# Kernel tuning notes

Hardware: AMD Instinct MI355X
Metric: run time of the kernel (lower is better)

The kernel has to match this reference:

```python
import jax, jax.numpy as jnp
import numpy as np

EPS = 1e-5

def _layer_norm(x, g, b):
    mu = jnp.mean(x, axis=-1, keepdims=True)
    var = jnp.mean((x - mu) ** 2, axis=-1, keepdims=True)
    return (x - mu) * jax.lax.rsqrt(var + EPS) * g + b

def _lstm(x, w_ih, w_hh, b_ih, b_hh):
    # x: [B,T,I]; w_ih: [4H,I]; w_hh: [4H,H]; gate order i,f,g,o (torch)
    B, T, _ = x.shape
    H = w_hh.shape[1]
    xg = jnp.einsum('bti,gi->btg', x, w_ih) + b_ih + b_hh  # [B,T,4H]
    def step(carry, xt):
        h, c = carry
        g = xt + h @ w_hh.T
        i, f, gg, o = jnp.split(g, 4, axis=-1)
        i = jax.nn.sigmoid(i); f = jax.nn.sigmoid(f)
        gg = jnp.tanh(gg); o = jax.nn.sigmoid(o)
        c = f * c + i * gg
        h = o * jnp.tanh(c)
        return (h, c), h
    h0 = jnp.zeros((B, H), x.dtype)
    (_, _), hs = jax.lax.scan(step, (h0, h0), jnp.swapaxes(xg, 0, 1))
    return jnp.swapaxes(hs, 0, 1)  # [B,T,H]

def _gru(x, w_ih, w_hh, b_ih, b_hh):
    # gate order r,z,n (torch); n uses r * (W_hn h + b_hn)
    B, T, _ = x.shape
    H = w_hh.shape[1]
    xg = jnp.einsum('bti,gi->btg', x, w_ih) + b_ih  # [B,T,3H]
    def step(h, xt):
        hg = h @ w_hh.T + b_hh
        xr, xz, xn = jnp.split(xt, 3, axis=-1)
        hr, hz, hn = jnp.split(hg, 3, axis=-1)
        r = jax.nn.sigmoid(xr + hr)
        z = jax.nn.sigmoid(xz + hz)
        n = jnp.tanh(xn + r * hn)
        h = (1.0 - z) * n + z * h
        return h, h
    h0 = jnp.zeros((B, H), x.dtype)
    _, hs = jax.lax.scan(step, h0, jnp.swapaxes(xg, 0, 1))
    return jnp.swapaxes(hs, 0, 1)

def _rnn_tanh(x, w_ih, w_hh, b_ih, b_hh):
    B, T, _ = x.shape
    H = w_hh.shape[1]
    xg = jnp.einsum('bti,gi->btg', x, w_ih) + b_ih + b_hh
    def step(h, xt):
        h = jnp.tanh(xt + h @ w_hh.T)
        return h, h
    h0 = jnp.zeros((B, H), x.dtype)
    _, hs = jax.lax.scan(step, h0, jnp.swapaxes(xg, 0, 1))
    return jnp.swapaxes(hs, 0, 1)

def setup_inputs() -> dict:
    key = jax.random.key(0)
    B, T, I, H, O = 32, 1024, 256, 512, 1000
    ks = jax.random.split(key, 16)
    s_lstm = 1.0 / np.sqrt(H)
    def u(k, shape, s):
        return jax.random.uniform(k, shape, jnp.float32, -s, s)
    return {
        'x': jax.random.normal(ks[0], (B, T, I), jnp.float32),
        'lstm_w_ih': u(ks[1], (4 * H, I), s_lstm),
        'lstm_w_hh': u(ks[2], (4 * H, H), s_lstm),
        'lstm_b_ih': u(ks[3], (4 * H,), s_lstm),
        'lstm_b_hh': u(ks[4], (4 * H,), s_lstm),
        'ln1_g': jnp.ones((H,), jnp.float32),
        'ln1_b': jnp.zeros((H,), jnp.float32),
        'gru_w_ih': u(ks[5], (3 * H, H), s_lstm),
        'gru_w_hh': u(ks[6], (3 * H, H), s_lstm),
        'gru_b_ih': u(ks[7], (3 * H,), s_lstm),
        'gru_b_hh': u(ks[8], (3 * H,), s_lstm),
        'ln2_g': jnp.ones((H,), jnp.float32),
        'ln2_b': jnp.zeros((H,), jnp.float32),
        'rnn_w_ih': u(ks[9], (H, H), s_lstm),
        'rnn_w_hh': u(ks[10], (H, H), s_lstm),
        'rnn_b_ih': u(ks[11], (H,), s_lstm),
        'rnn_b_hh': u(ks[12], (H,), s_lstm),
        'fc_w': u(ks[13], (O, H), s_lstm),
        'fc_b': u(ks[14], (O,), s_lstm),
    }

def reference(x, lstm_w_ih, lstm_w_hh, lstm_b_ih, lstm_b_hh, ln1_g, ln1_b,
              gru_w_ih, gru_w_hh, gru_b_ih, gru_b_hh, ln2_g, ln2_b,
              rnn_w_ih, rnn_w_hh, rnn_b_ih, rnn_b_hh, fc_w, fc_b):
    h = _lstm(x, lstm_w_ih, lstm_w_hh, lstm_b_ih, lstm_b_hh)
    h = _layer_norm(h, ln1_g, ln1_b)
    h = _gru(h, gru_w_ih, gru_w_hh, gru_b_ih, gru_b_hh)
    h = _layer_norm(h, ln2_g, ln2_b)
    h = _rnn_tanh(h, rnn_w_ih, rnn_w_hh, rnn_b_ih, rnn_b_hh)
    h = h[:, -1]  # [B,H]
    return h @ fc_w.T + fc_b  # [B,O]
```

## Files before the change

### kernel.cpp

```cpp
#include <hip/hip_runtime.h>
#include <stdint.h>

#define T_SEQ 1024
#define BATCH 32
#define HID   512
#define RING  32

typedef unsigned short u16;
typedef unsigned long long u64;
typedef short bf16x8 __attribute__((ext_vector_type(8)));
typedef float f32x4  __attribute__((ext_vector_type(4)));
typedef unsigned int u32x4 __attribute__((ext_vector_type(4)));

#define CAN64 0x7FC07FC07FC07FC0ull

__device__ __forceinline__ float bf2f(u16 u) {
  union { unsigned u; float f; } v; v.u = ((unsigned)u) << 16; return v.f;
}
__device__ __forceinline__ u16 f2bf(float f) {
  union { float f; unsigned u; } v; v.f = f;
  unsigned r = v.u + 0x7fffu + ((v.u >> 16) & 1u);
  return (u16)(r >> 16);
}
__device__ __forceinline__ float sigf(float x) { return 1.0f / (1.0f + __expf(-x)); }
__device__ __forceinline__ float tanh_fast(float x) { return 2.0f * sigf(2.0f * x) - 1.0f; }

__device__ __forceinline__ void st_dev(u64* p, u64 v) {
  __hip_atomic_store(p, v, __ATOMIC_RELAXED, __HIP_MEMORY_SCOPE_AGENT);
}
__device__ __forceinline__ int ld_flag(const int* p) {
  return __hip_atomic_load(p, __ATOMIC_RELAXED, __HIP_MEMORY_SCOPE_AGENT);
}

#define GLD16(dst, p, OFS) \
  asm volatile("global_load_dwordx4 %0, %1, off offset:" OFS " sc0 sc1" \
               : "=v"(dst) : "v"(p) : "memory")
#define GST16(p, val, OFS) \
  asm volatile("global_store_dwordx4 %0, %1, off offset:" OFS " sc0 sc1" \
               :: "v"(p), "v"(val) : "memory")

struct Frag {
  u32x4 d0,d1,d2,d3,d4,d5,d6,d7,d8,d9,d10,d11,d12,d13,d14,d15;
};

__device__ __forceinline__ void issue_frag(const u16* p, Frag& f) {
  GLD16(f.d0,  p, "0");   GLD16(f.d1,  p, "64");
  GLD16(f.d2,  p, "128"); GLD16(f.d3,  p, "192");
  GLD16(f.d4,  p, "256"); GLD16(f.d5,  p, "320");
  GLD16(f.d6,  p, "384"); GLD16(f.d7,  p, "448");
  GLD16(f.d8,  p, "512"); GLD16(f.d9,  p, "576");
  GLD16(f.d10, p, "640"); GLD16(f.d11, p, "704");
  GLD16(f.d12, p, "768"); GLD16(f.d13, p, "832");
  GLD16(f.d14, p, "896"); GLD16(f.d15, p, "960");
}

__device__ __forceinline__ bool chk16(u32x4 q) {
  union { u32x4 q; u64 h[2]; } u; u.q = q;
  return (u.h[0] != CAN64) & (u.h[1] != CAN64);
}
__device__ __forceinline__ bool frag_ok(const Frag& f) {
  bool ok = chk16(f.d0);
  ok &= chk16(f.d1);  ok &= chk16(f.d2);  ok &= chk16(f.d3);
  ok &= chk16(f.d4);  ok &= chk16(f.d5);  ok &= chk16(f.d6);
  ok &= chk16(f.d7);  ok &= chk16(f.d8);  ok &= chk16(f.d9);
  ok &= chk16(f.d10); ok &= chk16(f.d11); ok &= chk16(f.d12);
  ok &= chk16(f.d13); ok &= chk16(f.d14); ok &= chk16(f.d15);
  return ok;
}

__device__ __forceinline__ f32x4 frag_compute(const Frag& f, const u16 (*w)[520],
                                              int wrow, int kq) {
  f32x4 z = {0.f,0.f,0.f,0.f};
  f32x4 a[4] = {z, z, z, z};
#define FSTEP(ii, dd) { union { u32x4 q; bf16x8 v; } c; c.q = f.dd; \
  bf16x8 bv = *reinterpret_cast<const bf16x8*>(&w[wrow][kq + ii * 32]); \
  a[ii & 3] = __builtin_amdgcn_mfma_f32_16x16x32_bf16(c.v, bv, a[ii & 3], 0, 0, 0); }
  FSTEP(0,d0)   FSTEP(1,d1)   FSTEP(2,d2)   FSTEP(3,d3)
  FSTEP(4,d4)   FSTEP(5,d5)   FSTEP(6,d6)   FSTEP(7,d7)
  FSTEP(8,d8)   FSTEP(9,d9)   FSTEP(10,d10) FSTEP(11,d11)
  FSTEP(12,d12) FSTEP(13,d13) FSTEP(14,d14) FSTEP(15,d15)
#undef FSTEP
  return (a[0] + a[1]) + (a[2] + a[3]);
}

__device__ __forceinline__ int poll_min(const int* base, int n, int lane) {
  int f = 0x7fffffff;
  if (lane < n) f = ld_flag(&base[lane]);
#pragma unroll
  for (int off = 32; off >= 1; off >>= 1) {
    int o = __shfl_xor(f, off);
    f = o < f ? o : f;
  }
  return f;
}

__global__ __launch_bounds__(256) void cast_f32_bf16(const float* __restrict__ in,
                                                     u16* __restrict__ out, int n) {
  int i = (blockIdx.x * 256 + threadIdx.x) * 8;
  if (i + 7 < n) {
    float4 v0 = *reinterpret_cast<const float4*>(in + i);
    float4 v1 = *reinterpret_cast<const float4*>(in + i + 4);
    uint4 o;
    o.x = (unsigned)f2bf(v0.x) | ((unsigned)f2bf(v0.y) << 16);
    o.y = (unsigned)f2bf(v0.z) | ((unsigned)f2bf(v0.w) << 16);
    o.z = (unsigned)f2bf(v1.x) | ((unsigned)f2bf(v1.y) << 16);
    o.w = (unsigned)f2bf(v1.z) | ((unsigned)f2bf(v1.w) << 16);
    *reinterpret_cast<uint4*>(out + i) = o;
  } else {
    for (; i < n; ++i) out[i] = f2bf(in[i]);
  }
}

__global__ __launch_bounds__(256) void fill_canary(u64* __restrict__ p, long n) {
  long i = (long)blockIdx.x * 256 + threadIdx.x;
  if (i < n) p[i] = CAN64;
}

__global__ __launch_bounds__(256) void gemm_xg(
    const u16* __restrict__ A, const u16* __restrict__ W,
    const float* __restrict__ bias1, const float* __restrict__ bias2,
    u16* __restrict__ out, int N, int K, int strideB, int strideT)
{
  __shared__ u16 As[64][72];
  __shared__ u16 Bs[64][72];
  int tid  = threadIdx.x;
  int lane = tid & 63;
  int wave = tid >> 6;
  int m0 = blockIdx.x * 64;
  int n0 = blockIdx.y * 64;

  f32x4 zero = {0.f, 0.f, 0.f, 0.f};
  f32x4 acc[4] = {zero, zero, zero, zero};

  int srow = tid >> 2;
  int scol = (tid & 3) * 16;

  int m_s = m0 + srow;
  long arow = (long)(m_s & (BATCH - 1)) * strideB + (long)(m_s >> 5) * strideT;
  const u16* aptr = A + arow * K + scol;
  const u16* wptr = W + (long)(n0 + srow) * K + scol;

  for (int kk = 0; kk < K; kk += 64) {
    __syncthreads();
    uint4 a0 = *reinterpret_cast<const uint4*>(aptr + kk);
    uint4 a1 = *reinterpret_cast<const uint4*>(aptr + kk + 8);
    uint4 b0 = *reinterpret_cast<const uint4*>(wptr + kk);
    uint4 b1 = *reinterpret_cast<const uint4*>(wptr + kk + 8);
    *reinterpret_cast<uint4*>(&As[srow][scol])     = a0;
    *reinterpret_cast<uint4*>(&As[srow][scol + 8]) = a1;
    *reinterpret_cast<uint4*>(&Bs[srow][scol])     = b0;
    *reinterpret_cast<uint4*>(&Bs[srow][scol + 8]) = b1;
    __syncthreads();
    int am = wave * 16 + (lane & 15);
    int kq = (lane >> 4) * 8;
#pragma unroll
    for (int ks = 0; ks < 2; ++ks) {
      bf16x8 af = *reinterpret_cast<const bf16x8*>(&As[am][kq + ks * 32]);
#pragma unroll
      for (int nb = 0; nb < 4; ++nb) {
        bf16x8 bf = *reinterpret_cast<const bf16x8*>(&Bs[nb * 16 + (lane & 15)][kq + ks * 32]);
        acc[nb] = __builtin_amdgcn_mfma_f32_16x16x32_bf16(af, bf, acc[nb], 0, 0, 0);
      }
    }
  }
  int quad = lane >> 4;
#pragma unroll
  for (int nb = 0; nb < 4; ++nb) {
    int n = n0 + nb * 16 + (lane & 15);
    float bv = bias1[n] + (bias2 ? bias2[n] : 0.0f);
    int g = n >> 9, k = n & 511;
#pragma unroll
    for (int r = 0; r < 4; ++r) {
      int m = m0 + wave * 16 + quad * 4 + r;
      int t = m >> 5, b = m & (BATCH - 1);
      out[(((long)t * BATCH + b) * HID + k) * 4 + g] = f2bf(acc[nb][r] + bv);
    }
  }
}

template <int ROLE>
__device__ void recur_role(
    int wg, const u16* __restrict__ xg, const u16* __restrict__ up,
    const u16* __restrict__ wih, const u16* __restrict__ whh,
    const float* __restrict__ bih, const float* __restrict__ bhh,
    u16* __restrict__ hist, int* fl_own,
    const int* cons, int n_cons,
    u16 (*w_lds)[520], float (*gx)[33], float (*gh)[33], u16 (*hs)[8])
{
  constexpr int NG = (ROLE == 0) ? 4 : (ROLE == 1) ? 3 : 1;
  constexpr int NPAD = (ROLE == 2) ? 16 : 32;
  constexpr int XROWS = (ROLE > 0) ? NG * 8 : 0;
  constexpr int TOT = XROWS + NG * 8;
  int tid = threadIdx.x, lane = tid & 63, wave = tid >> 6;
  int hbase = wg * 8;

  for (int idx = tid; idx < TOT * 64; idx += 256) {
    int row = idx >> 6, chunk = idx & 63;
    int n = (row < XROWS) ? row : (row - XROWS);
    const u16* src = (row < XROWS) ? wih : whh;
    int g = n >> 3, dd = n & 7;
    uint4 v = *reinterpret_cast<const uint4*>(src + ((long)(g * 512 + hbase + dd)) * 512 + chunk * 8);
    *reinterpret_cast<uint4*>(&w_lds[row][chunk * 8]) = v;
  }
  __syncthreads();

  int mt = wave & 1, nt = wave >> 1;
  bool mact = (nt * 16) < NPAD;
  int colw = nt * 16 + (lane & 15);
  int wr = (colw < NG * 8) ? colw : (NG * 8 - 1);
  int arow = mt * 16 + (lane & 15);
  int kq = (lane >> 4) * 8;
  float bxw = 0.f, bhw = 0.f;
  if (colw < NG * 8) {
    int g = colw >> 3, dd = colw & 7;
    if constexpr (ROLE == 1) { bxw = bih[g * 512 + hbase + dd]; bhw = bhh[g * 512 + hbase + dd]; }
    if constexpr (ROLE == 2) { bxw = bih[hbase + dd] + bhh[hbase + dd]; }
    (void)g;
  }
  int b_c = tid >> 3, d_c = tid & 7;
  float c_st = 0.f, h_st = 0.f;
  int ccache = 0;

  for (int t = 0; t < T_SEQ; ++t) {
    u64 xq = 0;
    if constexpr (ROLE == 0)
      xq = *reinterpret_cast<const u64*>(xg + (((long)t * BATCH + b_c) * HID + hbase + d_c) * 4);

    f32x4 aX = {0.f,0.f,0.f,0.f}, aH = {0.f,0.f,0.f,0.f};
    if (mact) {
      if (wave == 0) {
        if (cons != nullptr && t >= RING - 1) {
          int need = t - (RING - 2);
          while (ccache < need) {
            ccache = poll_min(cons, n_cons, lane);
            if (ccache < need) __builtin_amdgcn_s_sleep(8);
          }
        }
        int pb = lane >> 1, half = lane & 1;
        st_dev(reinterpret_cast<u64*>(
                   hist + (((long)((t + 1) & (RING - 1)) * BATCH + pb) * HID + hbase + half * 4)),
               CAN64);
      }
      Frag fX, fH;
      bool okX = (ROLE == 0), okH = (t == 0);
      const u16* pX = nullptr;
      if constexpr (ROLE > 0)
        pX = up + ((long)(t & (RING - 1)) * BATCH + arow) * HID + kq;
      const u16* pH = hist + ((long)((t - 1) & (RING - 1)) * BATCH + arow) * HID + kq;
      while (!(okX & okH)) {
        if (!okX) issue_frag(pX, fX);
        if (!okH) issue_frag(pH, fH);
        asm volatile("s_waitcnt vmcnt(0)" ::: "memory");
        __builtin_amdgcn_sched_barrier(0);
        if (!okX) okX = (bool)__all(frag_ok(fX));
        if (!okH) okH = (bool)__all(frag_ok(fH));
      }
      if constexpr (ROLE > 0) aX = frag_compute(fX, w_lds, wr, kq);
      if (t > 0)              aH = frag_compute(fH, w_lds + XROWS, wr, kq);

      int quad = lane >> 4;
#pragma unroll
      for (int r = 0; r < 4; ++r) {
        int row = mt * 16 + quad * 4 + r;
        gx[row][colw] = aX[r] + bxw;
        gh[row][colw] = aH[r] + bhw;
      }
    }
    __syncthreads();

    float hnew;
    if constexpr (ROLE == 0) {
      float xv0 = bf2f((u16)(xq));
      float xv1 = bf2f((u16)(xq >> 16));
      float xv2 = bf2f((u16)(xq >> 32));
      float xv3 = bf2f((u16)(xq >> 48));
      float h0 = gh[b_c][0 * 8 + d_c];
      float h1 = gh[b_c][1 * 8 + d_c];
      float h2 = gh[b_c][2 * 8 + d_c];
      float h3 = gh[b_c][3 * 8 + d_c];
      float ig = sigf(xv0 + h0), fg = sigf(xv1 + h1);
      float gg = tanh_fast(xv2 + h2), og = sigf(xv3 + h3);
      c_st = fg * c_st + ig * gg;
      hnew = og * tanh_fast(c_st);
    } else if constexpr (ROLE == 1) {
      float xr_ = gx[b_c][0 * 8 + d_c], xz = gx[b_c][1 * 8 + d_c], xn = gx[b_c][2 * 8 + d_c];
      float hr  = gh[b_c][0 * 8 + d_c], hz = gh[b_c][1 * 8 + d_c], hn = gh[b_c][2 * 8 + d_c];
      float r = sigf(xr_ + hr), z = sigf(xz + hz);
      float n = tanh_fast(xn + r * hn);
      hnew = (1.f - z) * n + z * h_st;
      h_st = hnew;
    } else {
      hnew = tanh_fast(gx[b_c][d_c] + gh[b_c][d_c]);
    }
    hs[b_c][d_c] = f2bf(hnew);
    __syncthreads();

    if (wave == 0) {
      asm volatile("s_waitcnt vmcnt(0)" ::: "memory");
      int pb = lane >> 1, half = lane & 1;
      u64 val = *reinterpret_cast<const u64*>(&hs[pb][half * 4]);
      st_dev(reinterpret_cast<u64*>(
                 hist + (((long)(t & (RING - 1)) * BATCH + pb) * HID + hbase + half * 4)),
             val);
      if (tid == 0 && fl_own != nullptr)
        __hip_atomic_store(&fl_own[wg], t + 1, __ATOMIC_RELAXED, __HIP_MEMORY_SCOPE_AGENT);
    }
  }
}

__device__ void ln_role(int wg, const u16* __restrict__ in, u16* __restrict__ out,
                        const float* __restrict__ gv, const float* __restrict__ bv,
                        int* fl_out, const int* cons, int n_cons)
{
  int tid = threadIdx.x, lane = tid & 63, wave = tid >> 6;
  int row = wg * 8 + wave * 2 + (lane >> 5);
  int l32 = lane & 31, k0 = l32 * 16;
  float gr[16], br[16];
#pragma unroll
  for (int j = 0; j < 16; ++j) { gr[j] = gv[k0 + j]; br[j] = bv[k0 + j]; }
  int ccache = 0;
  u32x4 canv = {0x7FC07FC0u, 0x7FC07FC0u, 0x7FC07FC0u, 0x7FC07FC0u};

  for (int t = 0; t < T_SEQ; ++t) {
    if (t >= RING - 1) {
      int need = t - (RING - 2);
      while (ccache < need) {
        ccache = poll_min(cons, n_cons, lane);
        if (ccache < need) __builtin_amdgcn_s_sleep(8);
      }
    }
    u16* pc = out + ((long)((t + 1) & (RING - 1)) * BATCH + row) * HID + k0;
    GST16(pc, canv, "0");
    GST16(pc, canv, "16");

    const u16* p = in + ((long)(t & (RING - 1)) * BATCH + row) * HID + k0;
    u32x4 q0, q1;
    bool ok;
    do {
      GLD16(q0, p, "0");
      GLD16(q1, p, "16");
      asm volatile("s_waitcnt vmcnt(0)" ::: "memory");
      __builtin_amdgcn_sched_barrier(0);
      ok = (bool)__all(chk16(q0) & chk16(q1));
    } while (!ok);

    union { u32x4 q; u16 s[8]; } u0, u1;
    u0.q = q0; u1.q = q1;
    float x[16];
#pragma unroll
    for (int i = 0; i < 8; ++i) { x[i] = bf2f(u0.s[i]); x[8 + i] = bf2f(u1.s[i]); }
    float s = 0.f, s2 = 0.f;
#pragma unroll
    for (int i = 0; i < 16; ++i) { s += x[i]; s2 += x[i] * x[i]; }
#pragma unroll
    for (int off = 1; off < 32; off <<= 1) { s += __shfl_xor(s, off); s2 += __shfl_xor(s2, off); }
    float mu = s * (1.f / 512.f);
    float var = s2 * (1.f / 512.f) - mu * mu;
    float rs = rsqrtf(var + 1e-5f);
    union { u16 o[16]; u32x4 q[2]; } ov;
#pragma unroll
    for (int i = 0; i < 16; ++i) ov.o[i] = f2bf((x[i] - mu) * rs * gr[i] + br[i]);
    u16* po = out + ((long)(t & (RING - 1)) * BATCH + row) * HID + k0;
    GST16(po, ov.q[0], "0");
    GST16(po, ov.q[1], "16");
    __syncthreads();
    if (tid == 0)
      __hip_atomic_store(&fl_out[wg], t + 1, __ATOMIC_RELAXED, __HIP_MEMORY_SCOPE_AGENT);
  }
}

__global__ __launch_bounds__(256, 1) void fused_kernel(
    const u16* __restrict__ xg, const u16* __restrict__ lstm_whh,
    const u16* __restrict__ gru_wih, const u16* __restrict__ gru_whh,
    const float* __restrict__ gru_bih, const float* __restrict__ gru_bhh,
    const u16* __restrict__ rnn_wih, const u16* __restrict__ rnn_whh,
    const float* __restrict__ rnn_bih, const float* __restrict__ rnn_bhh,
    const float* __restrict__ ln1_g, const float* __restrict__ ln1_b,
    const float* __restrict__ ln2_g, const float* __restrict__ ln2_b,
    u16* h1, u16* ln1o, u16* h2, u16* ln2o, u16* h3, int* fl)
{
  __shared__ u16 w_lds[48][520];
  __shared__ float gx[32][33];
  __shared__ float gh[32][33];
  __shared__ u16 hs[32][8];
  int bid = blockIdx.x;
  if (bid < 64)
    recur_role<0>(bid, xg, nullptr, nullptr, lstm_whh, nullptr, nullptr,
                  h1, nullptr, fl + 64, 4, w_lds, gx, gh, hs);
  else if (bid < 68)
    ln_role(bid - 64, h1, ln1o, ln1_g, ln1_b, fl + 64, fl + 128, 64);
  else if (bid < 132)
    recur_role<1>(bid - 68, nullptr, ln1o, gru_wih, gru_whh, gru_bih, gru_bhh,
                  h2, fl + 128, fl + 192, 4, w_lds, gx, gh, hs);
  else if (bid < 136)
    ln_role(bid - 132, h2, ln2o, ln2_g, ln2_b, fl + 192, fl + 256, 64);
  else
    recur_role<2>(bid - 136, nullptr, ln2o, rnn_wih, rnn_whh, rnn_bih, rnn_bhh,
                  h3, fl + 256, nullptr, 0, w_lds, gx, gh, hs);
}

__global__ __launch_bounds__(256) void fc_kernel(
    const u16* __restrict__ hlast, const u16* __restrict__ w,
    const float* __restrict__ bias, float* __restrict__ out)
{
  int tg = blockIdx.x * 256 + threadIdx.x;
  if (tg >= BATCH * 1000) return;
  int b = tg / 1000, o = tg % 1000;
  const u16* hp = hlast + (long)b * HID;
  const u16* wp = w + (long)o * HID;
  float acc = 0.f;
  for (int k = 0; k < HID; k += 8) {
    uint4 hu = *reinterpret_cast<const uint4*>(hp + k);
    uint4 wu = *reinterpret_cast<const uint4*>(wp + k);
    u16* hsv = reinterpret_cast<u16*>(&hu);
    u16* wsv = reinterpret_cast<u16*>(&wu);
#pragma unroll
    for (int i = 0; i < 8; ++i) acc += bf2f(hsv[i]) * bf2f(wsv[i]);
  }
  out[tg] = acc + bias[o];
}

__global__ void sentinel_kernel(float* out) { out[0] = 12345.0f; }

extern "C" void kernel_launch(void* const* d_in, const int* in_sizes, int n_in,
                              void* d_out, int out_size, void* d_ws, size_t ws_size,
                              hipStream_t stream)
{
  (void)in_sizes; (void)n_in; (void)out_size;
  const float* x        = (const float*)d_in[0];
  const float* lstm_wih = (const float*)d_in[1];
  const float* lstm_whh = (const float*)d_in[2];
  const float* lstm_bih = (const float*)d_in[3];
  const float* lstm_bhh = (const float*)d_in[4];
  const float* ln1_g    = (const float*)d_in[5];
  const float* ln1_b    = (const float*)d_in[6];
  const float* gru_wih  = (const float*)d_in[7];
  const float* gru_whh  = (const float*)d_in[8];
  const float* gru_bih  = (const float*)d_in[9];
  const float* gru_bhh  = (const float*)d_in[10];
  const float* ln2_g    = (const float*)d_in[11];
  const float* ln2_b    = (const float*)d_in[12];
  const float* rnn_wih  = (const float*)d_in[13];
  const float* rnn_whh  = (const float*)d_in[14];
  const float* rnn_bih  = (const float*)d_in[15];
  const float* rnn_bhh  = (const float*)d_in[16];
  const float* fc_w     = (const float*)d_in[17];
  const float* fc_b     = (const float*)d_in[18];
  float* out = (float*)d_out;

  char* ws = (char*)d_ws;
  size_t off = 0;
  auto alloc = [&](size_t bytes) -> void* {
    void* p = ws + off; off += (bytes + 255) & ~(size_t)255; return p;
  };
  int* flags     = (int*)alloc(320 * sizeof(int));
  u16* xbf       = (u16*)alloc((size_t)BATCH * T_SEQ * 256 * 2);
  u16* lstm_wih_b= (u16*)alloc((size_t)2048 * 256 * 2);
  u16* lstm_whh_b= (u16*)alloc((size_t)2048 * 512 * 2);
  u16* gru_wih_b = (u16*)alloc((size_t)1536 * 512 * 2);
  u16* gru_whh_b = (u16*)alloc((size_t)1536 * 512 * 2);
  u16* rnn_wih_b = (u16*)alloc((size_t)512 * 512 * 2);
  u16* rnn_whh_b = (u16*)alloc((size_t)512 * 512 * 2);
  u16* fc_w_b    = (u16*)alloc((size_t)1000 * 512 * 2);
  u16* xg2       = (u16*)alloc((size_t)T_SEQ * BATCH * HID * 4 * 2);
  u16* h1        = (u16*)alloc((size_t)RING * BATCH * HID * 2);
  u16* ln1o      = (u16*)alloc((size_t)RING * BATCH * HID * 2);
  u16* h2        = (u16*)alloc((size_t)RING * BATCH * HID * 2);
  u16* ln2o      = (u16*)alloc((size_t)RING * BATCH * HID * 2);
  u16* h3        = (u16*)alloc((size_t)RING * BATCH * HID * 2);

  if (off > ws_size) {
    sentinel_kernel<<<1, 1, 0, stream>>>(out);
    return;
  }

  hipMemsetAsync(flags, 0, 320 * sizeof(int), stream);

  const long ncan = 5L * RING * BATCH * HID * 2 / 8;
  fill_canary<<<(int)((ncan + 255) / 256), 256, 0, stream>>>((u64*)h1, ncan);

  auto cast = [&](const float* src, u16* dst, int n) {
    cast_f32_bf16<<<(n + 2047) / 2048, 256, 0, stream>>>(src, dst, n);
  };
  cast(x,        xbf,        BATCH * T_SEQ * 256);
  cast(lstm_wih, lstm_wih_b, 2048 * 256);
  cast(lstm_whh, lstm_whh_b, 2048 * 512);
  cast(gru_wih,  gru_wih_b,  1536 * 512);
  cast(gru_whh,  gru_whh_b,  1536 * 512);
  cast(rnn_wih,  rnn_wih_b,  512 * 512);
  cast(rnn_whh,  rnn_whh_b,  512 * 512);
  cast(fc_w,     fc_w_b,     1000 * 512);

  const int M64 = (BATCH * T_SEQ) / 64;
  gemm_xg<<<dim3(M64, 2048 / 64), 256, 0, stream>>>(
      xbf, lstm_wih_b, lstm_bih, lstm_bhh, xg2, 2048, 256, 1024, 1);

  fused_kernel<<<200, 256, 0, stream>>>(
      xg2, lstm_whh_b,
      gru_wih_b, gru_whh_b, gru_bih, gru_bhh,
      rnn_wih_b, rnn_whh_b, rnn_bih, rnn_bhh,
      ln1_g, ln1_b, ln2_g, ln2_b,
      h1, ln1o, h2, ln2o, h3, flags);

  fc_kernel<<<(BATCH * 1000 + 255) / 256, 256, 0, stream>>>(
      h3 + (size_t)31 * BATCH * HID, fc_w_b, fc_b, out);
}
```

Before: 6.949 ms.

## Split recurrent matmul over K across waves and prefetch next-step input fragment

Reworks the per-step wave decomposition: instead of waves splitting over output columns (with some idle for the RNN role), each wave now takes half of the K dimension and all output columns, and partial sums are reduced through shared memory with an extra barrier. Fragments are halved to 8 loads, and the upstream input fragment for step t+1 is prefetched right after computing step t, so the input load latency overlaps the hidden-state wait. Biases move into the elementwise phase, and the trailing vmcnt wait before publishing h is dropped. Adds an extra __syncthreads and LDS accumulate per step, and relies on the prefetched sentinel check to retry stale data.

After: 6.273 ms. -9.7%, faster.

```diff
diff --git a/kernel.cpp b/kernel.cpp
--- a/kernel.cpp
+++ b/kernel.cpp
@@ -28,59 +28,52 @@
 __device__ __forceinline__ void st_dev(u64* p, u64 v) {
   __hip_atomic_store(p, v, __ATOMIC_RELAXED, __HIP_MEMORY_SCOPE_AGENT);
 }
+__device__ __forceinline__ void st_tag(int* p, int v) {
+  __hip_atomic_store(p, v, __ATOMIC_RELAXED, __HIP_MEMORY_SCOPE_AGENT);
+}
 __device__ __forceinline__ int ld_flag(const int* p) {
   return __hip_atomic_load(p, __ATOMIC_RELAXED, __HIP_MEMORY_SCOPE_AGENT);
 }
 
-#define GLD16(dst, p, OFS) \
+#define GLD16A(dst, p, OFS) \
   asm volatile("global_load_dwordx4 %0, %1, off offset:" OFS " sc0 sc1" \
                : "=v"(dst) : "v"(p) : "memory")
-#define GST16(p, val, OFS) \
+#define GST16A(p, val, OFS) \
   asm volatile("global_store_dwordx4 %0, %1, off offset:" OFS " sc0 sc1" \
                :: "v"(p), "v"(val) : "memory")
 
-struct Frag {
-  u32x4 d0,d1,d2,d3,d4,d5,d6,d7,d8,d9,d10,d11,d12,d13,d14,d15;
-};
-
-__device__ __forceinline__ void issue_frag(const u16* p, Frag& f) {
-  GLD16(f.d0,  p, "0");   GLD16(f.d1,  p, "64");
-  GLD16(f.d2,  p, "128"); GLD16(f.d3,  p, "192");
-  GLD16(f.d4,  p, "256"); GLD16(f.d5,  p, "320");
-  GLD16(f.d6,  p, "384"); GLD16(f.d7,  p, "448");
-  GLD16(f.d8,  p, "512"); GLD16(f.d9,  p, "576");
-  GLD16(f.d10, p, "640"); GLD16(f.d11, p, "704");
-  GLD16(f.d12, p, "768"); GLD16(f.d13, p, "832");
-  GLD16(f.d14, p, "896"); GLD16(f.d15, p, "960");
+struct Frag8 { u32x4 d0,d1,d2,d3,d4,d5,d6,d7; };
+
+__device__ __forceinline__ void issue_frag8A(const u16* p, Frag8& f) {
+  GLD16A(f.d0, p, "0");   GLD16A(f.d1, p, "64");
+  GLD16A(f.d2, p, "128"); GLD16A(f.d3, p, "192");
+  GLD16A(f.d4, p, "256"); GLD16A(f.d5, p, "320");
+  GLD16A(f.d6, p, "384"); GLD16A(f.d7, p, "448");
 }
 
 __device__ __forceinline__ bool chk16(u32x4 q) {
   union { u32x4 q; u64 h[2]; } u; u.q = q;
   return (u.h[0] != CAN64) & (u.h[1] != CAN64);
 }
-__device__ __forceinline__ bool frag_ok(const Frag& f) {
+__device__ __forceinline__ bool frag8_ok(const Frag8& f) {
   bool ok = chk16(f.d0);
-  ok &= chk16(f.d1);  ok &= chk16(f.d2);  ok &= chk16(f.d3);
-  ok &= chk16(f.d4);  ok &= chk16(f.d5);  ok &= chk16(f.d6);
-  ok &= chk16(f.d7);  ok &= chk16(f.d8);  ok &= chk16(f.d9);
-  ok &= chk16(f.d10); ok &= chk16(f.d11); ok &= chk16(f.d12);
-  ok &= chk16(f.d13); ok &= chk16(f.d14); ok &= chk16(f.d15);
+  ok &= chk16(f.d1); ok &= chk16(f.d2); ok &= chk16(f.d3);
+  ok &= chk16(f.d4); ok &= chk16(f.d5); ok &= chk16(f.d6); ok &= chk16(f.d7);
   return ok;
 }
 
-__device__ __forceinline__ f32x4 frag_compute(const Frag& f, const u16 (*w)[520],
-                                              int wrow, int kq) {
-  f32x4 z = {0.f,0.f,0.f,0.f};
-  f32x4 a[4] = {z, z, z, z};
-#define FSTEP(ii, dd) { union { u32x4 q; bf16x8 v; } c; c.q = f.dd; \
-  bf16x8 bv = *reinterpret_cast<const bf16x8*>(&w[wrow][kq + ii * 32]); \
-  a[ii & 3] = __builtin_amdgcn_mfma_f32_16x16x32_bf16(c.v, bv, a[ii & 3], 0, 0, 0); }
-  FSTEP(0,d0)   FSTEP(1,d1)   FSTEP(2,d2)   FSTEP(3,d3)
-  FSTEP(4,d4)   FSTEP(5,d5)   FSTEP(6,d6)   FSTEP(7,d7)
-  FSTEP(8,d8)   FSTEP(9,d9)   FSTEP(10,d10) FSTEP(11,d11)
-  FSTEP(12,d12) FSTEP(13,d13) FSTEP(14,d14) FSTEP(15,d15)
-#undef FSTEP
-  return (a[0] + a[1]) + (a[2] + a[3]);
+template <int NT>
+__device__ __forceinline__ void frag_compute8(const Frag8& f, const u16 (*w)[520],
+                                              int lane, int kq2, int ngr, f32x4* acc) {
+#define HSTEP(ii, dd) { union { u32x4 q; bf16x8 v; } c; c.q = f.dd; \
+  _Pragma("unroll") \
+  for (int n2 = 0; n2 < NT; ++n2) { \
+    int cw = n2 * 16 + (lane & 15); int wr2 = cw < ngr ? cw : ngr - 1; \
+    bf16x8 bv = *reinterpret_cast<const bf16x8*>(&w[wr2][kq2 + ii * 32]); \
+    acc[n2] = __builtin_amdgcn_mfma_f32_16x16x32_bf16(c.v, bv, acc[n2], 0, 0, 0); } }
+  HSTEP(0,d0) HSTEP(1,d1) HSTEP(2,d2) HSTEP(3,d3)
+  HSTEP(4,d4) HSTEP(5,d5) HSTEP(6,d6) HSTEP(7,d7)
+#undef HSTEP
 }
 
 __device__ __forceinline__ int poll_min(const int* base, int n, int lane) {
@@ -187,10 +180,12 @@
     const int* cons, int n_cons,
     u16 (*w_lds)[520], float (*gx)[33], float (*gh)[33], u16 (*hs)[8])
 {
-  constexpr int NG = (ROLE == 0) ? 4 : (ROLE == 1) ? 3 : 1;
-  constexpr int NPAD = (ROLE == 2) ? 16 : 32;
-  constexpr int XROWS = (ROLE > 0) ? NG * 8 : 0;
-  constexpr int TOT = XROWS + NG * 8;
+  constexpr int NG   = (ROLE == 0) ? 4 : (ROLE == 1) ? 3 : 1;
+  constexpr int NGR  = NG * 8;
+  constexpr int XROWS = (ROLE > 0) ? NGR : 0;
+  constexpr int TOT  = XROWS + NGR;
+  constexpr int NT   = (ROLE == 2) ? 1 : 2;
+  constexpr bool HASX = (ROLE > 0);
   int tid = threadIdx.x, lane = tid & 63, wave = tid >> 6;
   int hbase = wg * 8;
 
@@ -204,67 +199,101 @@
   }
   __syncthreads();
 
-  int mt = wave & 1, nt = wave >> 1;
-  bool mact = (nt * 16) < NPAD;
-  int colw = nt * 16 + (lane & 15);
-  int wr = (colw < NG * 8) ? colw : (NG * 8 - 1);
+  int mt = wave & 1, kh = wave >> 1;
   int arow = mt * 16 + (lane & 15);
-  int kq = (lane >> 4) * 8;
-  float bxw = 0.f, bhw = 0.f;
-  if (colw < NG * 8) {
-    int g = colw >> 3, dd = colw & 7;
-    if constexpr (ROLE == 1) { bxw = bih[g * 512 + hbase + dd]; bhw = bhh[g * 512 + hbase + dd]; }
-    if constexpr (ROLE == 2) { bxw = bih[hbase + dd] + bhh[hbase + dd]; }
-    (void)g;
-  }
+  int kq2  = kh * 256 + (lane >> 4) * 8;
+  int quad = lane >> 4;
   int b_c = tid >> 3, d_c = tid & 7;
   float c_st = 0.f, h_st = 0.f;
   int ccache = 0;
+  float bx0 = 0.f, bx1 = 0.f, bx2 = 0.f, bh0 = 0.f, bh1 = 0.f, bh2 = 0.f;
+  if constexpr (ROLE == 1) {
+    bx0 = bih[0 * 512 + hbase + d_c]; bx1 = bih[1 * 512 + hbase + d_c]; bx2 = bih[2 * 512 + hbase + d_c];
+    bh0 = bhh[0 * 512 + hbase + d_c]; bh1 = bhh[1 * 512 + hbase + d_c]; bh2 = bhh[2 * 512 + hbase + d_c];
+  }
+  if constexpr (ROLE == 2) bx0 = bih[hbase + d_c] + bhh[hbase + d_c];
+
+  Frag8 fXn;
+  if constexpr (HASX)
+    issue_frag8A(up + ((long)0 * BATCH + arow) * HID + kq2, fXn);
 
   for (int t = 0; t < T_SEQ; ++t) {
     u64 xq = 0;
     if constexpr (ROLE == 0)
       xq = *reinterpret_cast<const u64*>(xg + (((long)t * BATCH + b_c) * HID + hbase + d_c) * 4);
 
-    f32x4 aX = {0.f,0.f,0.f,0.f}, aH = {0.f,0.f,0.f,0.f};
-    if (mact) {
-      if (wave == 0) {
-        if (cons != nullptr && t >= RING - 1) {
-          int need = t - (RING - 2);
-          while (ccache < need) {
-            ccache = poll_min(cons, n_cons, lane);
-            if (ccache < need) __builtin_amdgcn_s_sleep(8);
-          }
+    if (wave == 0) {
+      if (cons != nullptr && t >= RING - 1) {
+        int need = t - (RING - 2);
+        while (ccache < need) {
+          ccache = poll_min(cons, n_cons, lane);
+          if (ccache < need) __builtin_amdgcn_s_sleep(8);
         }
-        int pb = lane >> 1, half = lane & 1;
-        st_dev(reinterpret_cast<u64*>(
-                   hist + (((long)((t + 1) & (RING - 1)) * BATCH + pb) * HID + hbase + half * 4)),
-               CAN64);
       }
-      Frag fX, fH;
-      bool okX = (ROLE == 0), okH = (t == 0);
-      const u16* pX = nullptr;
-      if constexpr (ROLE > 0)
-        pX = up + ((long)(t & (RING - 1)) * BATCH + arow) * HID + kq;
-      const u16* pH = hist + ((long)((t - 1) & (RING - 1)) * BATCH + arow) * HID + kq;
-      while (!(okX & okH)) {
-        if (!okX) issue_frag(pX, fX);
-        if (!okH) issue_frag(pH, fH);
+      int pb = lane >> 1, half = lane & 1;
+      st_dev(reinterpret_cast<u64*>(
+                 hist + (((long)((t + 1) & (RING - 1)) * BATCH + pb) * HID + hbase + half * 4)),
+             CAN64);
+    }
+
+    f32x4 zero4 = {0.f, 0.f, 0.f, 0.f};
+    f32x4 aXp[NT], aHp[NT];
+#pragma unroll
+    for (int n2 = 0; n2 < NT; ++n2) { aXp[n2] = zero4; aHp[n2] = zero4; }
+
+    Frag8 fH;
+    if (t > 0) {
+      const u16* pH = hist + ((long)((t - 1) & (RING - 1)) * BATCH + arow) * HID + kq2;
+      while (true) {
+        issue_frag8A(pH, fH);
         asm volatile("s_waitcnt vmcnt(0)" ::: "memory");
         __builtin_amdgcn_sched_barrier(0);
-        if (!okX) okX = (bool)__all(frag_ok(fX));
-        if (!okH) okH = (bool)__all(frag_ok(fH));
+        if (__all(frag8_ok(fH))) break;
+        __builtin_amdgcn_s_sleep(1);
       }
-      if constexpr (ROLE > 0) aX = frag_compute(fX, w_lds, wr, kq);
-      if (t > 0)              aH = frag_compute(fH, w_lds + XROWS, wr, kq);
-
-      int quad = lane >> 4;
-#pragma unroll
-      for (int r = 0; r < 4; ++r) {
-        int row = mt * 16 + quad * 4 + r;
-        gx[row][colw] = aX[r] + bxw;
-        gh[row][colw] = aH[r] + bhw;
+    } else {
+      asm volatile("s_waitcnt vmcnt(0)" ::: "memory");
+      __builtin_amdgcn_sched_barrier(0);
+    }
+
+    if constexpr (HASX) {
+      const u16* pX = up + ((long)(t & (RING - 1)) * BATCH + arow) * HID + kq2;
+      bool ok = (bool)__all(frag8_ok(fXn));
+      while (!ok) {
+        issue_frag8A(pX, fXn);
+        asm volatile("s_waitcnt vmcnt(0)" ::: "memory");
+        __builtin_amdgcn_sched_barrier(0);
+        ok = (bool)__all(frag8_ok(fXn));
+        if (!ok) __builtin_amdgcn_s_sleep(1);
       }
+      frag_compute8<NT>(fXn, w_lds, lane, kq2, NGR, aXp);
+      __builtin_amdgcn_sched_barrier(0);
+      if (t + 1 < T_SEQ)
+        issue_frag8A(up + ((long)((t + 1) & (RING - 1)) * BATCH + arow) * HID + kq2, fXn);
+    }
+    if (t > 0)
+      frag_compute8<NT>(fH, w_lds + XROWS, lane, kq2, NGR, aHp);
+
+    if (kh == 0) {
+#pragma unroll
+      for (int n2 = 0; n2 < NT; ++n2)
+#pragma unroll
+        for (int r = 0; r < 4; ++r) {
+          int row = mt * 16 + quad * 4 + r, col = n2 * 16 + (lane & 15);
+          if constexpr (HASX) gx[row][col] = aXp[n2][r];
+          gh[row][col] = aHp[n2][r];
+        }
+    }
+    __syncthreads();
+    if (kh == 1) {
+#pragma unroll
+      for (int n2 = 0; n2 < NT; ++n2)
+#pragma unroll
+        for (int r = 0; r < 4; ++r) {
+          int row = mt * 16 + quad * 4 + r, col = n2 * 16 + (lane & 15);
+          if constexpr (HASX) gx[row][col] += aXp[n2][r];
+          gh[row][col] += aHp[n2][r];
+        }
     }
     __syncthreads();
 
@@ -283,27 +312,30 @@
       c_st = fg * c_st + ig * gg;
       hnew = og * tanh_fast(c_st);
     } else if constexpr (ROLE == 1) {
-      float xr_ = gx[b_c][0 * 8 + d_c], xz = gx[b_c][1 * 8 + d_c], xn = gx[b_c][2 * 8 + d_c];
-      float hr  = gh[b_c][0 * 8 + d_c], hz = gh[b_c][1 * 8 + d_c], hn = gh[b_c][2 * 8 + d_c];
+      float xr_ = gx[b_c][0 * 8 + d_c] + bx0;
+      float xz  = gx[b_c][1 * 8 + d_c] + bx1;
+      float xn  = gx[b_c][2 * 8 + d_c] + bx2;
+      float hr  = gh[b_c][0 * 8 + d_c] + bh0;
+      float hz  = gh[b_c][1 * 8 + d_c] + bh1;
+      float hn  = gh[b_c][2 * 8 + d_c] + bh2;
       float r = sigf(xr_ + hr), z = sigf(xz + hz);
       float n = tanh_fast(xn + r * hn);
       hnew = (1.f - z) * n + z * h_st;
       h_st = hnew;
     } else {
-      hnew = tanh_fast(gx[b_c][d_c] + gh[b_c][d_c]);
+      hnew = tanh_fast(gx[b_c][d_c] + bx0 + gh[b_c][d_c]);
     }
     hs[b_c][d_c] = f2bf(hnew);
     __syncthreads();
 
     if (wave == 0) {
-      asm volatile("s_waitcnt vmcnt(0)" ::: "memory");
       int pb = lane >> 1, half = lane & 1;
       u64 val = *reinterpret_cast<const u64*>(&hs[pb][half * 4]);
       st_dev(reinterpret_cast<u64*>(
                  hist + (((long)(t & (RING - 1)) * BATCH + pb) * HID + hbase + half * 4)),
              val);
       if (tid == 0 && fl_own != nullptr)
-        __hip_atomic_store(&fl_own[wg], t + 1, __ATOMIC_RELAXED, __HIP_MEMORY_SCOPE_AGENT);
+        st_tag(&fl_own[wg], t + 1);
     }
   }
 }
@@ -330,15 +362,15 @@
       }
     }
     u16* pc = out + ((long)((t + 1) & (RING - 1)) * BATCH + row) * HID + k0;
-    GST16(pc, canv, "0");
-    GST16(pc, canv, "16");
+    GST16A(pc, canv, "0");
+    GST16A(pc, canv, "16");
 
     const u16* p = in + ((long)(t & (RING - 1)) * BATCH + row) * HID + k0;
     u32x4 q0, q1;
     bool ok;
     do {
-      GLD16(q0, p, "0");
-      GLD16(q1, p, "16");
+      GLD16A(q0, p, "0");
+      GLD16A(q1, p, "16");
       asm volatile("s_waitcnt vmcnt(0)" ::: "memory");
       __builtin_amdgcn_sched_barrier(0);
       ok = (bool)__all(chk16(q0) & chk16(q1));
@@ -361,11 +393,10 @@
 #pragma unroll
     for (int i = 0; i < 16; ++i) ov.o[i] = f2bf((x[i] - mu) * rs * gr[i] + br[i]);
     u16* po = out + ((long)(t & (RING - 1)) * BATCH + row) * HID + k0;
-    GST16(po, ov.q[0], "0");
-    GST16(po, ov.q[1], "16");
+    GST16A(po, ov.q[0], "0");
+    GST16A(po, ov.q[1], "16");
     __syncthreads();
-    if (tid == 0)
-      __hip_atomic_store(&fl_out[wg], t + 1, __ATOMIC_RELAXED, __HIP_MEMORY_SCOPE_AGENT);
+    if (tid == 0) st_tag(&fl_out[wg], t + 1);
   }
 }
 
```
